# Kernel tuning notes

Measured on AMD Instinct MI355X. Metric: run time of the kernel, lower is better.

Reference implementation:

```python
import jax, jax.numpy as jnp
import numpy as np
import math

D_MODEL = 512
NHEAD = 8
D_K = D_MODEL // NHEAD
WINDOW = 128
BATCH = 1
SEQ = 4096
NEG = -1e9  # matches torch masked_fill value


def setup_inputs() -> dict:
    key = jax.random.key(0)
    ks = jax.random.split(key, 9)
    s = 1.0 / math.sqrt(D_MODEL)
    return {
        "x": jax.random.normal(ks[0], (BATCH, SEQ, D_MODEL), dtype=jnp.float32),
        "wq": jax.random.uniform(ks[1], (D_MODEL, D_MODEL), jnp.float32, -s, s),
        "bq": jax.random.uniform(ks[2], (D_MODEL,), jnp.float32, -s, s),
        "wk": jax.random.uniform(ks[3], (D_MODEL, D_MODEL), jnp.float32, -s, s),
        "bk": jax.random.uniform(ks[4], (D_MODEL,), jnp.float32, -s, s),
        "wv": jax.random.uniform(ks[5], (D_MODEL, D_MODEL), jnp.float32, -s, s),
        "bv": jax.random.uniform(ks[6], (D_MODEL,), jnp.float32, -s, s),
        "wo": jax.random.uniform(ks[7], (D_MODEL, D_MODEL), jnp.float32, -s, s),
        "bo": jax.random.uniform(ks[8], (D_MODEL,), jnp.float32, -s, s),
    }


def reference(x, wq, bq, wk, bk, wv, bv, wo, bo):
    B, S, D = x.shape
    # projections -> (B, H, S, d_k)
    q = (x @ wq.T + bq).reshape(B, S, NHEAD, D_K).transpose(0, 2, 1, 3)
    k = (x @ wk.T + bk).reshape(B, S, NHEAD, D_K).transpose(0, 2, 1, 3)
    v = (x @ wv.T + bv).reshape(B, S, NHEAD, D_K).transpose(0, 2, 1, 3)
    # dense scores, band-masked (faithful to original: full S x S)
    scores = jnp.einsum('bhqd,bhkd->bhqk', q, k) / math.sqrt(D_K)
    idx = jnp.arange(S)
    band = jnp.abs(idx[:, None] - idx[None, :]) <= WINDOW  # (S, S)
    scores = jnp.where(band[None, None], scores, NEG)
    attn = jax.nn.softmax(scores, axis=-1)  # (B, H, S, S)
    ctx = jnp.einsum('bhqk,bhkd->bhqd', attn, v)
    ctx = ctx.transpose(0, 2, 1, 3).reshape(B, S, D)
    out = ctx @ wo.T + bo
    return out, attn
```

## Files before the change

kernel.cpp:

```cpp
#include <hip/hip_runtime.h>
#include <hip/hip_bf16.h>
#include <math.h>

#define S 4096
#define D 512
#define H 8
#define DK 64
#define WIN 128

typedef __attribute__((ext_vector_type(8))) short bf16x8;
typedef __attribute__((ext_vector_type(4))) float f32x4;

__device__ __forceinline__ unsigned short f2bf(float f) {
    __hip_bfloat16 h = __float2bfloat16(f);
    return *(unsigned short*)&h;
}

__global__ __launch_bounds__(256) void conv_bf16_kernel(
    const float* __restrict__ x,
    const float* __restrict__ wq, const float* __restrict__ wk,
    const float* __restrict__ wv, const float* __restrict__ wo,
    unsigned short* __restrict__ xb,
    unsigned short* __restrict__ wqb, unsigned short* __restrict__ wkb,
    unsigned short* __restrict__ wvb, unsigned short* __restrict__ wob)
{
    const float* src; unsigned short* dst; int n;
    switch (blockIdx.y) {
        case 0:  src = x;  dst = xb;  n = S * D; break;
        case 1:  src = wq; dst = wqb; n = D * D; break;
        case 2:  src = wk; dst = wkb; n = D * D; break;
        case 3:  src = wv; dst = wvb; n = D * D; break;
        default: src = wo; dst = wob; n = D * D; break;
    }
    const int i = (blockIdx.x * 256 + threadIdx.x) * 8;
    if (i >= n) return;
    float4 a = *(const float4*)&src[i];
    float4 b = *(const float4*)&src[i + 4];
    ushort4 o0 = {f2bf(a.x), f2bf(a.y), f2bf(a.z), f2bf(a.w)};
    ushort4 o1 = {f2bf(b.x), f2bf(b.y), f2bf(b.z), f2bf(b.w)};
    *(ushort4*)&dst[i]     = o0;
    *(ushort4*)&dst[i + 4] = o1;
}

__device__ __forceinline__ void mfma_gemm_body(
    const unsigned short* __restrict__ A,
    const unsigned short* __restrict__ W16,
    const float* __restrict__ bias,
    float* __restrict__ C,
    unsigned short* __restrict__ CB)
{
    __shared__ unsigned short Bs[64][520];

    const int tid  = threadIdx.x;
    const int m0   = blockIdx.x * 128;
    const int n0   = blockIdx.y * 64;
    const int wv   = tid >> 6;
    const int lane = tid & 63;
    const int l16  = lane & 15;
    const int klo  = (lane >> 4) * 8;

    #pragma unroll
    for (int it = 0; it < 16; ++it) {
        const int c   = tid + it * 256;
        const int row = c >> 6;
        const int kc  = (c & 63) * 8;
        *(bf16x8*)&Bs[row][kc] =
            *(const bf16x8*)&W16[(size_t)(n0 + row) * 512 + kc];
    }
    __syncthreads();

    const unsigned short* arow0 = &A[(size_t)(m0 + wv * 32 + l16) * 512 + klo];
    const unsigned short* arow1 = arow0 + 16 * 512;

    f32x4 acc[2][4];
    #pragma unroll
    for (int r = 0; r < 2; ++r)
        #pragma unroll
        for (int nf = 0; nf < 4; ++nf)
            acc[r][nf] = (f32x4){0.f, 0.f, 0.f, 0.f};

    #pragma unroll 4
    for (int kb = 0; kb < 512; kb += 32) {
        bf16x8 a0 = *(const bf16x8*)&arow0[kb];
        bf16x8 a1 = *(const bf16x8*)&arow1[kb];
        #pragma unroll
        for (int nf = 0; nf < 4; ++nf) {
            bf16x8 b = *(const bf16x8*)&Bs[nf * 16 + l16][kb + klo];
            acc[0][nf] = __builtin_amdgcn_mfma_f32_16x16x32_bf16(a0, b, acc[0][nf], 0, 0, 0);
            acc[1][nf] = __builtin_amdgcn_mfma_f32_16x16x32_bf16(a1, b, acc[1][nf], 0, 0, 0);
        }
    }

    const int r0 = (lane >> 4) * 4;
    #pragma unroll
    for (int r = 0; r < 2; ++r) {
        #pragma unroll
        for (int nf = 0; nf < 4; ++nf) {
            const int col = n0 + nf * 16 + l16;
            const float bb = bias[col];
            #pragma unroll
            for (int vv = 0; vv < 4; ++vv) {
                const int row = m0 + wv * 32 + r * 16 + r0 + vv;
                const float val = acc[r][nf][vv] + bb;
                if (C)  C [(size_t)row * 512 + col] = val;
                if (CB) CB[(size_t)row * 512 + col] = f2bf(val);
            }
        }
    }
}

__global__ __launch_bounds__(256) void proj3_kernel(
    const unsigned short* __restrict__ xb,
    const unsigned short* __restrict__ wqb, const float* __restrict__ bq,
    const unsigned short* __restrict__ wkb, const float* __restrict__ bk,
    const unsigned short* __restrict__ wvb, const float* __restrict__ bv,
    unsigned short* __restrict__ qb, unsigned short* __restrict__ kb,
    unsigned short* __restrict__ vb)
{
    const unsigned short* W; const float* b; unsigned short* CB;
    if (blockIdx.z == 0)      { W = wqb; b = bq; CB = qb; }
    else if (blockIdx.z == 1) { W = wkb; b = bk; CB = kb; }
    else                      { W = wvb; b = bv; CB = vb; }
    mfma_gemm_body(xb, W, b, nullptr, CB);
}

__global__ __launch_bounds__(256) void outproj_kernel(
    const unsigned short* __restrict__ ctxb,
    const unsigned short* __restrict__ wob, const float* __restrict__ bo,
    float* __restrict__ out)
{
    mfma_gemm_body(ctxb, wob, bo, out, nullptr);
}

__global__ __launch_bounds__(256) void band_attn_kernel(
    const unsigned short* __restrict__ qb, const unsigned short* __restrict__ kb,
    const unsigned short* __restrict__ vb,
    float* __restrict__ attn, unsigned short* __restrict__ ctxb)
{
    __shared__ __align__(16) unsigned short Qs[16][72];
    __shared__ __align__(16) unsigned short KV[64][72];
    __shared__ float P[16][336];
    __shared__ float rinvs[16];

    const int tid = threadIdx.x;
    const int h  = blockIdx.y;
    const int q0 = blockIdx.x * 16;
    const int w0 = q0 - 128;

    const int wv   = tid >> 6;
    const int lane = tid & 63;
    const int l16  = lane & 15;
    const int klo  = (lane >> 4) * 8;
    const int r0   = (lane >> 4) * 4;

    {
        const int row = tid >> 4;
        const int db  = (tid & 15) * 4;
        *(ushort4*)&Qs[row][db] =
            *(const ushort4*)&qb[(size_t)(q0 + row) * 512 + h * 64 + db];
    }

    const int lr = tid >> 2;
    const int ld = (tid & 3) * 16;

    for (int ch = 0; ch < 5; ++ch) {
        const int c0 = w0 + ch * 64;
        if (c0 + 64 <= 0 || c0 >= S) continue;
        __syncthreads();
        {
            const int krow = min(max(c0 + lr, 0), S - 1);
            const unsigned short* src = &kb[(size_t)krow * 512 + h * 64 + ld];
            *(bf16x8*)&KV[lr][ld]     = *(const bf16x8*)&src[0];
            *(bf16x8*)&KV[lr][ld + 8] = *(const bf16x8*)&src[8];
        }
        __syncthreads();

        f32x4 acc = (f32x4){0.f, 0.f, 0.f, 0.f};
        #pragma unroll
        for (int kk = 0; kk < 64; kk += 32) {
            bf16x8 a = *(const bf16x8*)&Qs[l16][kk + klo];
            bf16x8 b = *(const bf16x8*)&KV[wv * 16 + l16][kk + klo];
            acc = __builtin_amdgcn_mfma_f32_16x16x32_bf16(a, b, acc, 0, 0, 0);
        }
        #pragma unroll
        for (int vv = 0; vv < 4; ++vv)
            P[r0 + vv][ch * 64 + wv * 16 + l16] = acc[vv] * 0.125f;
    }
    __syncthreads();

    {
        const int r   = tid >> 4;
        const int lx  = tid & 15;
        const int i   = q0 + r;
        const int lo = max(i - WIN, 0) - w0;
        const int hi = min(i + WIN, S - 1) - w0;

        float m = -1e30f;
        for (int c = lo + lx; c <= hi; c += 16) m = fmaxf(m, P[r][c]);
        m = fmaxf(m, __shfl_xor(m, 1));
        m = fmaxf(m, __shfl_xor(m, 2));
        m = fmaxf(m, __shfl_xor(m, 4));
        m = fmaxf(m, __shfl_xor(m, 8));

        float sum = 0.f;
        for (int c = lx; c < 320; c += 16) {
            float e = 0.f;
            if (c >= lo && c <= hi) {
                e = __expf(P[r][c] - m);
                sum += e;
            }
            P[r][c] = e;
        }
        sum += __shfl_xor(sum, 1);
        sum += __shfl_xor(sum, 2);
        sum += __shfl_xor(sum, 4);
        sum += __shfl_xor(sum, 8);
        if (lx == 0) rinvs[r] = 1.0f / sum;
    }

    f32x4 pacc = (f32x4){0.f, 0.f, 0.f, 0.f};
    for (int ch = 0; ch < 5; ++ch) {
        const int c0 = w0 + ch * 64;
        if (c0 + 64 <= 0 || c0 >= S) continue;
        __syncthreads();
        {
            const int vrow = min(max(c0 + lr, 0), S - 1);
            ushort4 v0 = *(const ushort4*)&vb[(size_t)vrow * 512 + h * 64 + ld];
            ushort4 v1 = *(const ushort4*)&vb[(size_t)vrow * 512 + h * 64 + ld + 4];
            ushort4 v2 = *(const ushort4*)&vb[(size_t)vrow * 512 + h * 64 + ld + 8];
            ushort4 v3 = *(const ushort4*)&vb[(size_t)vrow * 512 + h * 64 + ld + 12];
            KV[ld +  0][lr] = v0.x; KV[ld +  1][lr] = v0.y;
            KV[ld +  2][lr] = v0.z; KV[ld +  3][lr] = v0.w;
            KV[ld +  4][lr] = v1.x; KV[ld +  5][lr] = v1.y;
            KV[ld +  6][lr] = v1.z; KV[ld +  7][lr] = v1.w;
            KV[ld +  8][lr] = v2.x; KV[ld +  9][lr] = v2.y;
            KV[ld + 10][lr] = v2.z; KV[ld + 11][lr] = v2.w;
            KV[ld + 12][lr] = v3.x; KV[ld + 13][lr] = v3.y;
            KV[ld + 14][lr] = v3.z; KV[ld + 15][lr] = v3.w;
        }
        __syncthreads();

        #pragma unroll
        for (int kk = 0; kk < 64; kk += 32) {
            unsigned short abuf[8];
            #pragma unroll
            for (int e = 0; e < 8; ++e)
                abuf[e] = f2bf(P[l16][ch * 64 + kk + klo + e]);
            bf16x8 a = *(const bf16x8*)abuf;
            bf16x8 b = *(const bf16x8*)&KV[wv * 16 + l16][kk + klo];
            pacc = __builtin_amdgcn_mfma_f32_16x16x32_bf16(a, b, pacc, 0, 0, 0);
        }
    }

    #pragma unroll
    for (int vv = 0; vv < 4; ++vv) {
        const int row = q0 + r0 + vv;
        ctxb[(size_t)row * 512 + h * 64 + wv * 16 + l16] =
            f2bf(pacc[vv] * rinvs[r0 + vv]);
    }

    float* rowbase = attn + (size_t)h * S * S;
    #pragma unroll 1
    for (int r = 0; r < 16; ++r) {
        const int i = q0 + r;
        float* rowp = rowbase + (size_t)i * S;
        const int lo = max(i - WIN, 0) - w0;
        const int hi = min(i + WIN, S - 1) - w0;
        const float rv = rinvs[r];
        #pragma unroll
        for (int t = 0; t < 4; ++t) {
            const int c4 = (tid + t * 256) << 2;
            const int lc = c4 - w0;
            float4 o;
            if (lc >= lo && lc + 3 <= hi) {
                float4 p = *(const float4*)&P[r][lc];
                o.x = p.x * rv; o.y = p.y * rv; o.z = p.z * rv; o.w = p.w * rv;
            } else if (lc + 3 < lo || lc > hi) {
                o = make_float4(0.f, 0.f, 0.f, 0.f);
            } else {
                o.x = (lc + 0 >= lo && lc + 0 <= hi) ? P[r][lc + 0] * rv : 0.f;
                o.y = (lc + 1 >= lo && lc + 1 <= hi) ? P[r][lc + 1] * rv : 0.f;
                o.z = (lc + 2 >= lo && lc + 2 <= hi) ? P[r][lc + 2] * rv : 0.f;
                o.w = (lc + 3 >= lo && lc + 3 <= hi) ? P[r][lc + 3] * rv : 0.f;
            }
            *(float4*)&rowp[c4] = o;
        }
    }
}

extern "C" void kernel_launch(void* const* d_in, const int* in_sizes, int n_in,
                              void* d_out, int out_size, void* d_ws, size_t ws_size,
                              hipStream_t stream)
{
    (void)in_sizes; (void)n_in; (void)out_size; (void)ws_size;
    const float* x  = (const float*)d_in[0];
    const float* wq = (const float*)d_in[1];
    const float* bq = (const float*)d_in[2];
    const float* wk = (const float*)d_in[3];
    const float* bk = (const float*)d_in[4];
    const float* wv = (const float*)d_in[5];
    const float* bv = (const float*)d_in[6];
    const float* wo = (const float*)d_in[7];
    const float* bo = (const float*)d_in[8];

    float* out  = (float*)d_out;
    float* attn = out + (size_t)S * D;

    unsigned short* xb   = (unsigned short*)d_ws;
    unsigned short* qb   = xb   + (size_t)S * D;
    unsigned short* kb   = qb   + (size_t)S * D;
    unsigned short* vb   = kb   + (size_t)S * D;
    unsigned short* ctxb = vb   + (size_t)S * D;
    unsigned short* wqb  = ctxb + (size_t)S * D;
    unsigned short* wkb  = wqb  + (size_t)D * D;
    unsigned short* wvb  = wkb  + (size_t)D * D;
    unsigned short* wob  = wvb  + (size_t)D * D;

    conv_bf16_kernel<<<dim3(1024, 5), 256, 0, stream>>>(
        x, wq, wk, wv, wo, xb, wqb, wkb, wvb, wob);
    proj3_kernel<<<dim3(32, 8, 3), 256, 0, stream>>>(
        xb, wqb, bq, wkb, bk, wvb, bv, qb, kb, vb);
    band_attn_kernel<<<dim3(256, 8), 256, 0, stream>>>(qb, kb, vb, attn, ctxb);
    outproj_kernel<<<dim3(32, 8), 256, 0, stream>>>(ctxb, wob, bo, out);
}
```

Measured before the change: 146.8 us.

## Pre-transpose V and feed band-attention MFMAs directly from global memory

Adds a small kernel that writes V transposed per head, so each row of vT is one head dimension laid out along the sequence. The band-attention kernel drops its LDS staging of Q, K and V and their barriers. Q and K fragments are loaded straight into registers, and V fragments come as contiguous 8-element loads from vT. P is now read as vector float4 values before conversion to bf16. This removes the scalar transposing LDS stores and the per-chunk synchronisation. The cost is an extra kernel launch, an extra workspace buffer, and uncoalesced per-lane global loads for K.

```diff
diff --git a/kernel.cpp b/kernel.cpp
--- a/kernel.cpp
+++ b/kernel.cpp
@@ -40,6 +40,26 @@
     ushort4 o1 = {f2bf(b.x), f2bf(b.y), f2bf(b.z), f2bf(b.w)};
     *(ushort4*)&dst[i]     = o0;
     *(ushort4*)&dst[i + 4] = o1;
+}
+
+__global__ __launch_bounds__(256) void vtrans_kernel(
+    const unsigned short* __restrict__ vb, unsigned short* __restrict__ vT)
+{
+    __shared__ unsigned short T[64][72];
+    const int tid = threadIdx.x;
+    const int s0 = blockIdx.x * 64;
+    const int h  = blockIdx.y;
+    const int r = tid >> 2;
+    const int c = (tid & 3) * 16;
+    *(bf16x8*)&T[r][c]     = *(const bf16x8*)&vb[(size_t)(s0 + r) * 512 + h * 64 + c];
+    *(bf16x8*)&T[r][c + 8] = *(const bf16x8*)&vb[(size_t)(s0 + r) * 512 + h * 64 + c + 8];
+    __syncthreads();
+    unsigned short o[16];
+    #pragma unroll
+    for (int e = 0; e < 16; ++e) o[e] = T[c + e][r];
+    unsigned short* dst = &vT[((size_t)h * 64 + r) * 4096 + s0 + c];
+    *(bf16x8*)&dst[0] = *(bf16x8*)&o[0];
+    *(bf16x8*)&dst[8] = *(bf16x8*)&o[8];
 }
 
 __device__ __forceinline__ void mfma_gemm_body(
@@ -134,12 +154,10 @@
 
 __global__ __launch_bounds__(256) void band_attn_kernel(
     const unsigned short* __restrict__ qb, const unsigned short* __restrict__ kb,
-    const unsigned short* __restrict__ vb,
+    const unsigned short* __restrict__ vT,
     float* __restrict__ attn, unsigned short* __restrict__ ctxb)
 {
-    __shared__ __align__(16) unsigned short Qs[16][72];
-    __shared__ __align__(16) unsigned short KV[64][72];
-    __shared__ float P[16][336];
+    __shared__ float P[16][340];
     __shared__ float rinvs[16];
 
     const int tid = threadIdx.x;
@@ -153,35 +171,20 @@
     const int klo  = (lane >> 4) * 8;
     const int r0   = (lane >> 4) * 4;
 
-    {
-        const int row = tid >> 4;
-        const int db  = (tid & 15) * 4;
-        *(ushort4*)&Qs[row][db] =
-            *(const ushort4*)&qb[(size_t)(q0 + row) * 512 + h * 64 + db];
-    }
-
-    const int lr = tid >> 2;
-    const int ld = (tid & 3) * 16;
+    const unsigned short* qrow = &qb[(size_t)(q0 + l16) * 512 + h * 64 + klo];
+    const bf16x8 aq0 = *(const bf16x8*)&qrow[0];
+    const bf16x8 aq1 = *(const bf16x8*)&qrow[32];
 
     for (int ch = 0; ch < 5; ++ch) {
         const int c0 = w0 + ch * 64;
         if (c0 + 64 <= 0 || c0 >= S) continue;
-        __syncthreads();
-        {
-            const int krow = min(max(c0 + lr, 0), S - 1);
-            const unsigned short* src = &kb[(size_t)krow * 512 + h * 64 + ld];
-            *(bf16x8*)&KV[lr][ld]     = *(const bf16x8*)&src[0];
-            *(bf16x8*)&KV[lr][ld + 8] = *(const bf16x8*)&src[8];
-        }
-        __syncthreads();
-
+        const int krow = min(max(c0 + wv * 16 + l16, 0), S - 1);
+        const unsigned short* krp = &kb[(size_t)krow * 512 + h * 64 + klo];
+        bf16x8 b0 = *(const bf16x8*)&krp[0];
+        bf16x8 b1 = *(const bf16x8*)&krp[32];
         f32x4 acc = (f32x4){0.f, 0.f, 0.f, 0.f};
-        #pragma unroll
-        for (int kk = 0; kk < 64; kk += 32) {
-            bf16x8 a = *(const bf16x8*)&Qs[l16][kk + klo];
-            bf16x8 b = *(const bf16x8*)&KV[wv * 16 + l16][kk + klo];
-            acc = __builtin_amdgcn_mfma_f32_16x16x32_bf16(a, b, acc, 0, 0, 0);
-        }
+        acc = __builtin_amdgcn_mfma_f32_16x16x32_bf16(aq0, b0, acc, 0, 0, 0);
+        acc = __builtin_amdgcn_mfma_f32_16x16x32_bf16(aq1, b1, acc, 0, 0, 0);
         #pragma unroll
         for (int vv = 0; vv < 4; ++vv)
             P[r0 + vv][ch * 64 + wv * 16 + l16] = acc[vv] * 0.125f;
@@ -217,37 +220,23 @@
         sum += __shfl_xor(sum, 8);
         if (lx == 0) rinvs[r] = 1.0f / sum;
     }
+    __syncthreads();
 
     f32x4 pacc = (f32x4){0.f, 0.f, 0.f, 0.f};
+    const unsigned short* vtrow = &vT[((size_t)h * 64 + wv * 16 + l16) * 4096];
     for (int ch = 0; ch < 5; ++ch) {
         const int c0 = w0 + ch * 64;
         if (c0 + 64 <= 0 || c0 >= S) continue;
-        __syncthreads();
-        {
-            const int vrow = min(max(c0 + lr, 0), S - 1);
-            ushort4 v0 = *(const ushort4*)&vb[(size_t)vrow * 512 + h * 64 + ld];
-            ushort4 v1 = *(const ushort4*)&vb[(size_t)vrow * 512 + h * 64 + ld + 4];
-            ushort4 v2 = *(const ushort4*)&vb[(size_t)vrow * 512 + h * 64 + ld + 8];
-            ushort4 v3 = *(const ushort4*)&vb[(size_t)vrow * 512 + h * 64 + ld + 12];
-            KV[ld +  0][lr] = v0.x; KV[ld +  1][lr] = v0.y;
-            KV[ld +  2][lr] = v0.z; KV[ld +  3][lr] = v0.w;
-            KV[ld +  4][lr] = v1.x; KV[ld +  5][lr] = v1.y;
-            KV[ld +  6][lr] = v1.z; KV[ld +  7][lr] = v1.w;
-            KV[ld +  8][lr] = v2.x; KV[ld +  9][lr] = v2.y;
-            KV[ld + 10][lr] = v2.z; KV[ld + 11][lr] = v2.w;
-            KV[ld + 12][lr] = v3.x; KV[ld + 13][lr] = v3.y;
-            KV[ld + 14][lr] = v3.z; KV[ld + 15][lr] = v3.w;
-        }
-        __syncthreads();
-
         #pragma unroll
         for (int kk = 0; kk < 64; kk += 32) {
-            unsigned short abuf[8];
-            #pragma unroll
-            for (int e = 0; e < 8; ++e)
-                abuf[e] = f2bf(P[l16][ch * 64 + kk + klo + e]);
-            bf16x8 a = *(const bf16x8*)abuf;
-            bf16x8 b = *(const bf16x8*)&KV[wv * 16 + l16][kk + klo];
+            f32x4 p0 = *(const f32x4*)&P[l16][ch * 64 + kk + klo];
+            f32x4 p1 = *(const f32x4*)&P[l16][ch * 64 + kk + klo + 4];
+            unsigned short ab[8] = {f2bf(p0[0]), f2bf(p0[1]), f2bf(p0[2]), f2bf(p0[3]),
+                                    f2bf(p1[0]), f2bf(p1[1]), f2bf(p1[2]), f2bf(p1[3])};
+            bf16x8 a = *(const bf16x8*)ab;
+            int offs = c0 + kk + klo;
+            offs = min(max(offs, 0), S - 8);
+            bf16x8 b = *(const bf16x8*)&vtrow[offs];
             pacc = __builtin_amdgcn_mfma_f32_16x16x32_bf16(a, b, pacc, 0, 0, 0);
         }
     }
@@ -311,7 +300,8 @@
     unsigned short* kb   = qb   + (size_t)S * D;
     unsigned short* vb   = kb   + (size_t)S * D;
     unsigned short* ctxb = vb   + (size_t)S * D;
-    unsigned short* wqb  = ctxb + (size_t)S * D;
+    unsigned short* vT   = ctxb + (size_t)S * D;
+    unsigned short* wqb  = vT   + (size_t)S * D;
     unsigned short* wkb  = wqb  + (size_t)D * D;
     unsigned short* wvb  = wkb  + (size_t)D * D;
     unsigned short* wob  = wvb  + (size_t)D * D;
@@ -320,6 +310,7 @@
         x, wq, wk, wv, wo, xb, wqb, wkb, wvb, wob);
     proj3_kernel<<<dim3(32, 8, 3), 256, 0, stream>>>(
         xb, wqb, bq, wkb, bk, wvb, bv, qb, kb, vb);
-    band_attn_kernel<<<dim3(256, 8), 256, 0, stream>>>(qb, kb, vb, attn, ctxb);
+    vtrans_kernel<<<dim3(64, 8), 256, 0, stream>>>(vb, vT);
+    band_attn_kernel<<<dim3(256, 8), 256, 0, stream>>>(qb, kb, vT, attn, ctxb);
     outproj_kernel<<<dim3(32, 8), 256, 0, stream>>>(ctxb, wob, bo, out);
 }
```

After: 152.6 us. +3.9%, slower.
